# Performance work log

Measured on AMD Instinct MI355X. Metric: run time of the kernel, lower is better.

Reference implementation:

```python
import jax, jax.numpy as jnp
import numpy as np

EDGE_DROPOUT_RATE = 0.5  # RGCNEncoder edge_dropout_rate
DROPOUT_KEY = 42         # fixed key standing in for the encoder's dropout_key


def setup_inputs() -> dict:
    key = jax.random.key(0)
    ks = jax.random.split(key, 6)
    N, R, E, D, B, BI, BO = 100000, 16, 50000, 500, 100, 5, 5
    x = 0.01 * jax.random.normal(ks[0], (N, D), dtype=jnp.float32)  # pre_transform, normal() init (stddev=0.01)
    # block-decomposed relation weights: R relations x 100 blocks of 5x5
    w_rel1 = jax.random.normal(ks[1], (R, B, BI, BO), dtype=jnp.float32) / np.sqrt(BI)
    w_self1 = jax.random.normal(ks[2], (D, D), dtype=jnp.float32) / np.sqrt(D)
    w_rel2 = jax.random.normal(ks[3], (R, B, BI, BO), dtype=jnp.float32) / np.sqrt(BI)
    w_self2 = jax.random.normal(ks[4], (D, D), dtype=jnp.float32) / np.sqrt(D)
    edge_type_idcs = jax.random.randint(ks[5], (R, 2, E), 0, N, dtype=jnp.int32)
    edge_masks = jnp.ones((R, E), dtype=bool)
    return {"x": x, "w_rel1": w_rel1, "w_self1": w_self1,
            "w_rel2": w_rel2, "w_self2": w_self2,
            "edge_type_idcs": edge_type_idcs, "edge_masks": edge_masks}


def _rgcn_layer(h, w_rel, w_self, edge_type_idcs, edge_mask_f):
    """One block-decomposed RGCNConv with per-relation-node normalization + self loop."""
    N = h.shape[0]
    R, B, BI, BO = w_rel.shape
    Dout = B * BO
    out = h @ w_self  # self-connection
    for r in range(R):  # small fixed set of relations
        src = edge_type_idcs[r, 0]
        dst = edge_type_idcs[r, 1]
        mr = edge_mask_f[r]                              # [E]
        E = src.shape[0]
        hs = h[src].reshape(E, B, BI)                    # gather + split into blocks
        msg = jnp.einsum('ebi,bio->ebo', hs, w_rel[r]).reshape(E, Dout)
        msg = msg * mr[:, None]                          # masked (incl. edge dropout)
        agg = jax.ops.segment_sum(msg, dst, num_segments=N)   # [N, Dout]
        cnt = jax.ops.segment_sum(mr, dst, num_segments=N)    # per-relation in-degree
        out = out + agg / jnp.maximum(cnt, 1.0)[:, None]
    return jax.nn.relu(out)


def reference(x, w_rel1, w_self1, w_rel2, w_self2, edge_type_idcs, edge_masks):
    # edge dropout (all_data.dropout): keep each edge with prob 1 - rate
    keep = jax.random.bernoulli(jax.random.key(DROPOUT_KEY), 1.0 - EDGE_DROPOUT_RATE, edge_masks.shape)
    mask_f = (edge_masks & keep).astype(x.dtype)
    h = _rgcn_layer(x, w_rel1, w_self1, edge_type_idcs, mask_f)
    h = _rgcn_layer(h, w_rel2, w_self2, edge_type_idcs, mask_f)
    return h
```

## Files before the change

### kernel.cpp

```cpp
#include <hip/hip_runtime.h>
#include <hip/hip_bf16.h>
#include <stdint.h>

#define N_NODES 100000
#define N_REL   16
#define N_EDGE  50000
#define DIM     500
#define TOT_E   (N_REL * N_EDGE)
#define CNT_N   (N_REL * N_NODES)

#define INV_OFF    0ull
#define DEG_OFF    6400000ull
#define ROW_OFF    6800000ull
#define SCANP_OFF  7201000ull
#define CURS_OFF   7210000ull
#define ELIST_OFF  7610000ull
#define WB1_OFF    14020000ull
#define WB2_OFF    14550000ull
#define H1_OFF     15080000ull
#define WEXP1_OFF  115080000ull
#define WEXP2_OFF  115240000ull

typedef __attribute__((ext_vector_type(8))) short bf16x8;
typedef __attribute__((ext_vector_type(4))) float f32x4;

__device__ __forceinline__ uint32_t rotl32(uint32_t x, int d) {
    return (x << d) | (x >> (32 - d));
}
__device__ __forceinline__ bool edge_keep(uint32_t j) {
    uint32_t x0 = 0u, x1 = j;
    const uint32_t ks0 = 0u, ks1 = 42u, ks2 = 0u ^ 42u ^ 0x1BD11BDAu;
    const int RA[4] = {13, 15, 26, 6};
    const int RB[4] = {17, 29, 16, 24};
    x0 += ks0; x1 += ks1;
#pragma unroll
    for (int i = 0; i < 4; i++) { x0 += x1; x1 = rotl32(x1, RA[i]); x1 ^= x0; }
    x0 += ks1; x1 += ks2 + 1u;
#pragma unroll
    for (int i = 0; i < 4; i++) { x0 += x1; x1 = rotl32(x1, RB[i]); x1 ^= x0; }
    x0 += ks2; x1 += ks0 + 2u;
#pragma unroll
    for (int i = 0; i < 4; i++) { x0 += x1; x1 = rotl32(x1, RA[i]); x1 ^= x0; }
    x0 += ks0; x1 += ks1 + 3u;
#pragma unroll
    for (int i = 0; i < 4; i++) { x0 += x1; x1 = rotl32(x1, RB[i]); x1 ^= x0; }
    x0 += ks1; x1 += ks2 + 4u;
#pragma unroll
    for (int i = 0; i < 4; i++) { x0 += x1; x1 = rotl32(x1, RA[i]); x1 ^= x0; }
    x0 += ks2; x1 += ks0 + 5u;
    return ((x0 ^ x1) >> 31) == 0u;
}

__device__ __forceinline__ uint16_t f2bf(float f) {
    uint32_t u = __float_as_uint(f);
    u += 0x7FFFu + ((u >> 16) & 1u);
    return (uint16_t)(u >> 16);
}
__device__ __forceinline__ float bf2f(uint16_t v) {
    return __uint_as_float((uint32_t)v << 16);
}

__global__ __launch_bounds__(256) void zero_kernel(uint32_t* __restrict__ p, int n) {
    int t = blockIdx.x * blockDim.x + threadIdx.x;
    if (t < n) p[t] = 0u;
}

__global__ __launch_bounds__(256) void count_kernel(
        const int* __restrict__ eidx, uint32_t* __restrict__ cnt,
        uint32_t* __restrict__ deg) {
    int tid = blockIdx.x * blockDim.x + threadIdx.x;
    if (tid >= TOT_E) return;
    if (edge_keep((uint32_t)tid)) {
        int r = tid / N_EDGE;
        int e = tid - r * N_EDGE;
        int dst = eidx[(r * 2 + 1) * N_EDGE + e];
        atomicAdd(&cnt[r * N_NODES + dst], 1u);
        atomicAdd(&deg[dst], 1u);
    }
}

__global__ __launch_bounds__(256) void inv_kernel(uint32_t* __restrict__ cnt_u,
                                                  float* __restrict__ inv) {
    int t = blockIdx.x * blockDim.x + threadIdx.x;
    if (t < CNT_N) {
        float c = (float)cnt_u[t];
        inv[t] = 1.0f / fmaxf(c, 1.0f);
    }
}

__global__ __launch_bounds__(256) void scan1_kernel(
        const uint32_t* __restrict__ deg, uint32_t* __restrict__ rowptr,
        uint32_t* __restrict__ scanp) {
    __shared__ uint32_t sh[256];
    int b = blockIdx.x, t = threadIdx.x;
    int base = b * 1024 + t * 4;
    uint32_t x[4];
#pragma unroll
    for (int i = 0; i < 4; i++) x[i] = (base + i < N_NODES) ? deg[base + i] : 0u;
    uint32_t s = x[0] + x[1] + x[2] + x[3];
    sh[t] = s; __syncthreads();
    for (int off = 1; off < 256; off <<= 1) {
        uint32_t v = (t >= off) ? sh[t - off] : 0u;
        __syncthreads();
        sh[t] += v;
        __syncthreads();
    }
    uint32_t run = sh[t] - s;
    if (t == 255) scanp[b] = sh[255];
#pragma unroll
    for (int i = 0; i < 4; i++) {
        if (base + i < N_NODES) rowptr[base + i] = run;
        run += x[i];
    }
}

__global__ __launch_bounds__(128) void scan2_kernel(
        uint32_t* __restrict__ scanp, uint32_t* __restrict__ rowptr, int nb) {
    __shared__ uint32_t sh[128];
    int t = threadIdx.x;
    uint32_t v = (t < nb) ? scanp[t] : 0u;
    sh[t] = v; __syncthreads();
    for (int off = 1; off < 128; off <<= 1) {
        uint32_t u = (t >= off) ? sh[t - off] : 0u;
        __syncthreads();
        sh[t] += u;
        __syncthreads();
    }
    if (t < nb) scanp[t] = sh[t] - v;
    if (t == 127) rowptr[N_NODES] = sh[127];
}

__global__ __launch_bounds__(256) void scan3_kernel(
        uint32_t* __restrict__ rowptr, const uint32_t* __restrict__ scanp,
        uint32_t* __restrict__ curs) {
    int b = blockIdx.x, t = threadIdx.x;
    int base = b * 1024 + t * 4;
    uint32_t off = scanp[b];
#pragma unroll
    for (int i = 0; i < 4; i++) {
        int idx = base + i;
        if (idx < N_NODES) {
            uint32_t v = rowptr[idx] + off;
            rowptr[idx] = v;
            curs[idx] = v;
        }
    }
}

__global__ __launch_bounds__(256) void scatter_kernel(
        const int* __restrict__ eidx, const float* __restrict__ inv,
        uint32_t* __restrict__ curs, uint2* __restrict__ elist2) {
    int tid = blockIdx.x * blockDim.x + threadIdx.x;
    if (tid >= TOT_E) return;
    if (edge_keep((uint32_t)tid)) {
        int r = tid / N_EDGE;
        int e = tid - r * N_EDGE;
        int src = eidx[(r * 2 + 0) * N_EDGE + e];
        int dst = eidx[(r * 2 + 1) * N_EDGE + e];
        uint32_t pos = atomicAdd(&curs[dst], 1u);
        uint2 rec;
        rec.x = (uint32_t)src | ((uint32_t)r << 20);
        rec.y = __float_as_uint(inv[r * N_NODES + dst]);
        elist2[pos] = rec;
    }
}

__global__ __launch_bounds__(256) void conv_x_kernel(
        const float4* __restrict__ in, ushort4* __restrict__ outp, int n4) {
    int t = blockIdx.x * blockDim.x + threadIdx.x;
    if (t >= n4) return;
    float4 v = in[t];
    ushort4 o;
    o.x = f2bf(v.x); o.y = f2bf(v.y); o.z = f2bf(v.z); o.w = f2bf(v.w);
    outp[t] = o;
}

__global__ __launch_bounds__(256) void conv_w_kernel(
        const float* __restrict__ W, uint16_t* __restrict__ Bt) {
    int idx = blockIdx.x * 256 + threadIdx.x;
    int n = idx >> 9, k = idx & 511;
    float v = (n < DIM && k < DIM) ? W[k * DIM + n] : 0.f;
    Bt[idx] = f2bf(v);
}

__global__ __launch_bounds__(256) void conv_wexp_kernel(
        const float* __restrict__ W, float* __restrict__ wexp) {
    int idx = blockIdx.x * 256 + threadIdx.x;
    if (idx >= N_REL * 5 * DIM) return;
    int r = idx / (5 * DIM);
    int rem = idx - r * 5 * DIM;
    int i = rem / DIM;
    int j = rem - i * DIM;
    wexp[idx] = W[r * 2500 + (j / 5) * 25 + i * 5 + (j % 5)];
}

__global__ __launch_bounds__(256) void gemm_mfma_kernel(
        const uint16_t* __restrict__ A, const uint16_t* __restrict__ Bt,
        float* __restrict__ C, int M) {
    __shared__ uint16_t As[64][72];
    __shared__ uint16_t Bs[64][72];
    int m0 = blockIdx.x * 64;
    int n0 = blockIdx.y * 64;
    int t = threadIdx.x;
    int wave = t >> 6, lane = t & 63;
    int row_s = t >> 2;
    int k4 = (t & 3) * 16;
    f32x4 acc[4] = {};

    for (int k0 = 0; k0 < 512; k0 += 64) {
        {
            int gm = m0 + row_s;
            int gk = k0 + k4;
            uint16_t* dst = &As[row_s][k4];
            if (gm < M && gk + 15 < DIM) {
                *(bf16x8*)dst       = *(const bf16x8*)&A[(long)gm * DIM + gk];
                *(bf16x8*)(dst + 8) = *(const bf16x8*)&A[(long)gm * DIM + gk + 8];
            } else {
#pragma unroll
                for (int i = 0; i < 16; i++)
                    dst[i] = (gm < M && gk + i < DIM) ? A[(long)gm * DIM + gk + i] : (uint16_t)0;
            }
        }
        {
            uint16_t* dst = &Bs[row_s][k4];
            const uint16_t* srcp = &Bt[(n0 + row_s) * 512 + k0 + k4];
            *(bf16x8*)dst       = *(const bf16x8*)srcp;
            *(bf16x8*)(dst + 8) = *(const bf16x8*)(srcp + 8);
        }
        __syncthreads();

        int rA = (wave << 4) + (lane & 15);
        int ks = (lane >> 4) * 8;
        bf16x8 a0 = *(const bf16x8*)&As[rA][ks];
        bf16x8 a1 = *(const bf16x8*)&As[rA][32 + ks];
#pragma unroll
        for (int nt = 0; nt < 4; nt++) {
            int cB = (nt << 4) + (lane & 15);
            bf16x8 b0 = *(const bf16x8*)&Bs[cB][ks];
            bf16x8 b1 = *(const bf16x8*)&Bs[cB][32 + ks];
            acc[nt] = __builtin_amdgcn_mfma_f32_16x16x32_bf16(a0, b0, acc[nt], 0, 0, 0);
            acc[nt] = __builtin_amdgcn_mfma_f32_16x16x32_bf16(a1, b1, acc[nt], 0, 0, 0);
        }
        __syncthreads();
    }

    int rbase = m0 + (wave << 4) + ((lane >> 4) << 2);
    int cl = lane & 15;
#pragma unroll
    for (int nt = 0; nt < 4; nt++) {
        int col = n0 + (nt << 4) + cl;
        if (col < DIM) {
#pragma unroll
            for (int q = 0; q < 4; q++) {
                int rr = rbase + q;
                if (rr < M) C[(long)rr * DIM + col] = acc[nt][q];
            }
        }
    }
}

template <bool BF16H, bool OUT_BF16>
__global__ __launch_bounds__(256) void gather_kernel(
        const void* __restrict__ h, const float* __restrict__ wexp,
        const uint2* __restrict__ elist2, const uint32_t* __restrict__ rowptr,
        const float* __restrict__ self_in, float* __restrict__ out_f32,
        uint16_t* __restrict__ out_bf16) {
    int n = blockIdx.x;
    int wv = threadIdx.x >> 6, l = threadIdx.x & 63;
    const int D0 = wv * 125;
    const int j0 = l, j1 = l + 64;
    const bool has1 = (j1 < 125);
    const int b0 = j0 / 5;
    const int b1 = j1 / 5;

    __shared__ float hsb[4][2][128];

    uint32_t s = rowptr[n], e = rowptr[n + 1];
    float a0 = 0.f, a1 = 0.f;

    for (uint32_t p = s; p < e; p += 4) {
        const int k = (int)min(4u, e - p);
        uint2 rec[4];
#pragma unroll
        for (int i = 0; i < 4; i++) {
            if (i < k) rec[i] = elist2[p + i];
        }
        float v0[4], v1[4];
#pragma unroll
        for (int i = 0; i < 4; i++) {
            if (i < k) {
                uint32_t src = rec[i].x & 0xFFFFFu;
                if constexpr (BF16H) {
                    const uint16_t* row = (const uint16_t*)h + (size_t)src * DIM + D0;
                    v0[i] = bf2f(row[j0]);
                    v1[i] = has1 ? bf2f(row[j1]) : 0.f;
                } else {
                    const float* row = (const float*)h + (size_t)src * DIM + D0;
                    v0[i] = row[j0];
                    v1[i] = has1 ? row[j1] : 0.f;
                }
            }
        }
#pragma unroll
        for (int i = 0; i < 4; i++) {
            if (i < k) {
                float* hs = hsb[wv][i & 1];
                hs[j0] = v0[i];
                if (has1) hs[j1] = v1[i];
                uint32_t rl = rec[i].x >> 20;
                float inv = __uint_as_float(rec[i].y);
                const float* wbase = wexp + (size_t)rl * (5 * DIM) + D0;
                float w0[5];
#pragma unroll
                for (int q = 0; q < 5; q++) w0[q] = wbase[q * DIM + j0];
                const float* hp0 = hs + b0 * 5;
                float d0 = hp0[0] * w0[0] + hp0[1] * w0[1] + hp0[2] * w0[2]
                         + hp0[3] * w0[3] + hp0[4] * w0[4];
                a0 = fmaf(inv, d0, a0);
                if (has1) {
                    float w1[5];
#pragma unroll
                    for (int q = 0; q < 5; q++) w1[q] = wbase[q * DIM + j1];
                    const float* hp1 = hs + b1 * 5;
                    float d1 = hp1[0] * w1[0] + hp1[1] * w1[1] + hp1[2] * w1[2]
                             + hp1[3] * w1[3] + hp1[4] * w1[4];
                    a1 = fmaf(inv, d1, a1);
                }
            }
        }
    }

    long ob = (long)n * DIM + D0;
    {
        float v = fmaxf(self_in[ob + j0] + a0, 0.f);
        if (OUT_BF16) out_bf16[ob + j0] = f2bf(v);
        else          out_f32[ob + j0] = v;
    }
    if (has1) {
        float v = fmaxf(self_in[ob + j1] + a1, 0.f);
        if (OUT_BF16) out_bf16[ob + j1] = f2bf(v);
        else          out_f32[ob + j1] = v;
    }
}

extern "C" void kernel_launch(void* const* d_in, const int* in_sizes, int n_in,
                              void* d_out, int out_size, void* d_ws, size_t ws_size,
                              hipStream_t stream) {
    const float* x       = nullptr;
    const float* w_rel1  = nullptr;
    const float* w_rel2  = nullptr;
    const float* w_self1 = nullptr;
    const float* w_self2 = nullptr;
    const int*   eidx    = nullptr;
    for (int i = 0; i < n_in; i++) {
        int s = in_sizes[i];
        if (s == N_NODES * DIM) {
            x = (const float*)d_in[i];
        } else if (s == N_REL * 100 * 25) {
            if (!w_rel1) w_rel1 = (const float*)d_in[i];
            else         w_rel2 = (const float*)d_in[i];
        } else if (s == DIM * DIM) {
            if (!w_self1) w_self1 = (const float*)d_in[i];
            else          w_self2 = (const float*)d_in[i];
        } else if (s == N_REL * 2 * N_EDGE) {
            eidx = (const int*)d_in[i];
        }
    }
    float* out = (float*)d_out;

    char* ws = (char*)d_ws;
    uint32_t* cnt_u  = (uint32_t*)(ws + INV_OFF);
    float*    inv    = (float*)(ws + INV_OFF);
    uint32_t* deg    = (uint32_t*)(ws + DEG_OFF);
    uint32_t* rowptr = (uint32_t*)(ws + ROW_OFF);
    uint32_t* scanp  = (uint32_t*)(ws + SCANP_OFF);
    uint32_t* curs   = (uint32_t*)(ws + CURS_OFF);
    uint2*    elist2 = (uint2*)(ws + ELIST_OFF);
    uint16_t* wb1    = (uint16_t*)(ws + WB1_OFF);
    uint16_t* wb2    = (uint16_t*)(ws + WB2_OFF);
    uint16_t* h1     = (uint16_t*)(ws + H1_OFF);
    float*    wexp1  = (float*)(ws + WEXP1_OFF);
    float*    wexp2  = (float*)(ws + WEXP2_OFF);

    const int NB = (N_NODES + 1023) / 1024;

    zero_kernel<<<(CNT_N + N_NODES + 255) / 256, 256, 0, stream>>>(cnt_u, CNT_N + N_NODES);
    count_kernel<<<(TOT_E + 255) / 256, 256, 0, stream>>>(eidx, cnt_u, deg);
    inv_kernel<<<(CNT_N + 255) / 256, 256, 0, stream>>>(cnt_u, inv);
    scan1_kernel<<<NB, 256, 0, stream>>>(deg, rowptr, scanp);
    scan2_kernel<<<1, 128, 0, stream>>>(scanp, rowptr, NB);
    scan3_kernel<<<NB, 256, 0, stream>>>(rowptr, scanp, curs);
    scatter_kernel<<<(TOT_E + 255) / 256, 256, 0, stream>>>(eidx, inv, curs, elist2);

    conv_x_kernel<<<(N_NODES * DIM / 4 + 255) / 256, 256, 0, stream>>>(
        (const float4*)x, (ushort4*)h1, N_NODES * DIM / 4);
    conv_w_kernel<<<512 * 512 / 256, 256, 0, stream>>>(w_self1, wb1);
    conv_w_kernel<<<512 * 512 / 256, 256, 0, stream>>>(w_self2, wb2);
    conv_wexp_kernel<<<(N_REL * 5 * DIM + 255) / 256, 256, 0, stream>>>(w_rel1, wexp1);
    conv_wexp_kernel<<<(N_REL * 5 * DIM + 255) / 256, 256, 0, stream>>>(w_rel2, wexp2);

    dim3 ggrid((N_NODES + 63) / 64, 8);

    gemm_mfma_kernel<<<ggrid, 256, 0, stream>>>(h1, wb1, out, N_NODES);
    gather_kernel<false, true><<<N_NODES, 256, 0, stream>>>(
        x, wexp1, elist2, rowptr, out, nullptr, h1);

    gemm_mfma_kernel<<<ggrid, 256, 0, stream>>>(h1, wb2, out, N_NODES);
    gather_kernel<true, false><<<N_NODES, 256, 0, stream>>>(
        h1, wexp2, elist2, rowptr, out, out, nullptr);
}
```

Measured before the change: 1.225 ms.

## Enlarge self-GEMM tiles to 128x128 with 2x2 wave layout; prefetch self term

The dense self-connection GEMM now uses 128x128 output tiles, with each of four waves computing a 64x64 sub-tile as a 4x4 grid of MFMA fragments. This cuts how often A and B tiles are reloaded from global memory, raises the MFMA-to-load ratio, and halves the grid's column dimension. The cost is many more accumulator registers per thread and more LDS per block, which may lower occupancy. The gather kernel also loads its self-term value at the start so that load overlaps the edge loop.

```diff
diff --git a/kernel.cpp b/kernel.cpp
--- a/kernel.cpp
+++ b/kernel.cpp
@@ -194,66 +194,78 @@
     wexp[idx] = W[r * 2500 + (j / 5) * 25 + i * 5 + (j % 5)];
 }
 
-__global__ __launch_bounds__(256) void gemm_mfma_kernel(
+__global__ __launch_bounds__(256) void gemm_mfma128_kernel(
         const uint16_t* __restrict__ A, const uint16_t* __restrict__ Bt,
         float* __restrict__ C, int M) {
-    __shared__ uint16_t As[64][72];
-    __shared__ uint16_t Bs[64][72];
-    int m0 = blockIdx.x * 64;
-    int n0 = blockIdx.y * 64;
+    __shared__ uint16_t As[128][72];
+    __shared__ uint16_t Bs[128][72];
+    int m0 = blockIdx.x * 128;
+    int n0 = blockIdx.y * 128;
     int t = threadIdx.x;
     int wave = t >> 6, lane = t & 63;
-    int row_s = t >> 2;
-    int k4 = (t & 3) * 16;
-    f32x4 acc[4] = {};
+    int wm = wave >> 1, wn = wave & 1;
+    f32x4 acc[4][4] = {};
 
     for (int k0 = 0; k0 < 512; k0 += 64) {
-        {
-            int gm = m0 + row_s;
-            int gk = k0 + k4;
-            uint16_t* dst = &As[row_s][k4];
-            if (gm < M && gk + 15 < DIM) {
-                *(bf16x8*)dst       = *(const bf16x8*)&A[(long)gm * DIM + gk];
-                *(bf16x8*)(dst + 8) = *(const bf16x8*)&A[(long)gm * DIM + gk + 8];
+#pragma unroll
+        for (int i = 0; i < 4; i++) {
+            int c = t * 4 + i;
+            int row = c >> 3;
+            int col = (c & 7) * 8;
+            int gm = m0 + row, gk = k0 + col;
+            uint16_t* dst = &As[row][col];
+            if (gm < M && gk + 7 < DIM) {
+                *(bf16x8*)dst = *(const bf16x8*)&A[(size_t)gm * DIM + gk];
             } else {
 #pragma unroll
-                for (int i = 0; i < 16; i++)
-                    dst[i] = (gm < M && gk + i < DIM) ? A[(long)gm * DIM + gk + i] : (uint16_t)0;
+                for (int q = 0; q < 8; q++)
+                    dst[q] = (gm < M && gk + q < DIM) ? A[(size_t)gm * DIM + gk + q]
+                                                      : (uint16_t)0;
             }
-        }
-        {
-            uint16_t* dst = &Bs[row_s][k4];
-            const uint16_t* srcp = &Bt[(n0 + row_s) * 512 + k0 + k4];
-            *(bf16x8*)dst       = *(const bf16x8*)srcp;
-            *(bf16x8*)(dst + 8) = *(const bf16x8*)(srcp + 8);
-        }
-        __syncthreads();
-
-        int rA = (wave << 4) + (lane & 15);
+            *(bf16x8*)&Bs[row][col] =
+                *(const bf16x8*)&Bt[(size_t)(n0 + row) * 512 + k0 + col];
+        }
+        __syncthreads();
+
         int ks = (lane >> 4) * 8;
-        bf16x8 a0 = *(const bf16x8*)&As[rA][ks];
-        bf16x8 a1 = *(const bf16x8*)&As[rA][32 + ks];
+        int rl = lane & 15;
+        bf16x8 af[4][2], bfr[4][2];
+#pragma unroll
+        for (int mt = 0; mt < 4; mt++) {
+            af[mt][0] = *(const bf16x8*)&As[wm * 64 + mt * 16 + rl][ks];
+            af[mt][1] = *(const bf16x8*)&As[wm * 64 + mt * 16 + rl][32 + ks];
+        }
 #pragma unroll
         for (int nt = 0; nt < 4; nt++) {
-            int cB = (nt << 4) + (lane & 15);
-            bf16x8 b0 = *(const bf16x8*)&Bs[cB][ks];
-            bf16x8 b1 = *(const bf16x8*)&Bs[cB][32 + ks];
-            acc[nt] = __builtin_amdgcn_mfma_f32_16x16x32_bf16(a0, b0, acc[nt], 0, 0, 0);
-            acc[nt] = __builtin_amdgcn_mfma_f32_16x16x32_bf16(a1, b1, acc[nt], 0, 0, 0);
-        }
-        __syncthreads();
-    }
-
-    int rbase = m0 + (wave << 4) + ((lane >> 4) << 2);
+            bfr[nt][0] = *(const bf16x8*)&Bs[wn * 64 + nt * 16 + rl][ks];
+            bfr[nt][1] = *(const bf16x8*)&Bs[wn * 64 + nt * 16 + rl][32 + ks];
+        }
+#pragma unroll
+        for (int mt = 0; mt < 4; mt++)
+#pragma unroll
+            for (int nt = 0; nt < 4; nt++) {
+                acc[mt][nt] = __builtin_amdgcn_mfma_f32_16x16x32_bf16(
+                    af[mt][0], bfr[nt][0], acc[mt][nt], 0, 0, 0);
+                acc[mt][nt] = __builtin_amdgcn_mfma_f32_16x16x32_bf16(
+                    af[mt][1], bfr[nt][1], acc[mt][nt], 0, 0, 0);
+            }
+        __syncthreads();
+    }
+
     int cl = lane & 15;
-#pragma unroll
-    for (int nt = 0; nt < 4; nt++) {
-        int col = n0 + (nt << 4) + cl;
-        if (col < DIM) {
-#pragma unroll
-            for (int q = 0; q < 4; q++) {
-                int rr = rbase + q;
-                if (rr < M) C[(long)rr * DIM + col] = acc[nt][q];
+    int rq = (lane >> 4) << 2;
+#pragma unroll
+    for (int mt = 0; mt < 4; mt++) {
+        int rbase = m0 + wm * 64 + mt * 16 + rq;
+#pragma unroll
+        for (int nt = 0; nt < 4; nt++) {
+            int col = n0 + wn * 64 + nt * 16 + cl;
+            if (col < DIM) {
+#pragma unroll
+                for (int q = 0; q < 4; q++) {
+                    int rr = rbase + q;
+                    if (rr < M) C[(size_t)rr * DIM + col] = acc[mt][nt][q];
+                }
             }
         }
     }
@@ -275,6 +287,10 @@
 
     __shared__ float hsb[4][2][128];
 
+    long ob = (long)n * DIM + D0;
+    float self0 = self_in[ob + j0];
+    float self1 = has1 ? self_in[ob + j1] : 0.f;
+
     uint32_t s = rowptr[n], e = rowptr[n + 1];
     float a0 = 0.f, a1 = 0.f;
 
@@ -330,14 +346,13 @@
         }
     }
 
-    long ob = (long)n * DIM + D0;
     {
-        float v = fmaxf(self_in[ob + j0] + a0, 0.f);
+        float v = fmaxf(self0 + a0, 0.f);
         if (OUT_BF16) out_bf16[ob + j0] = f2bf(v);
         else          out_f32[ob + j0] = v;
     }
     if (has1) {
-        float v = fmaxf(self_in[ob + j1] + a1, 0.f);
+        float v = fmaxf(self1 + a1, 0.f);
         if (OUT_BF16) out_bf16[ob + j1] = f2bf(v);
         else          out_f32[ob + j1] = v;
     }
@@ -399,13 +414,13 @@
     conv_wexp_kernel<<<(N_REL * 5 * DIM + 255) / 256, 256, 0, stream>>>(w_rel1, wexp1);
     conv_wexp_kernel<<<(N_REL * 5 * DIM + 255) / 256, 256, 0, stream>>>(w_rel2, wexp2);
 
-    dim3 ggrid((N_NODES + 63) / 64, 8);
-
-    gemm_mfma_kernel<<<ggrid, 256, 0, stream>>>(h1, wb1, out, N_NODES);
+    dim3 ggrid((N_NODES + 127) / 128, 4);
+
+    gemm_mfma128_kernel<<<ggrid, 256, 0, stream>>>(h1, wb1, out, N_NODES);
     gather_kernel<false, true><<<N_NODES, 256, 0, stream>>>(
         x, wexp1, elist2, rowptr, out, nullptr, h1);
 
-    gemm_mfma_kernel<<<ggrid, 256, 0, stream>>>(h1, wb2, out, N_NODES);
+    gemm_mfma128_kernel<<<ggrid, 256, 0, stream>>>(h1, wb2, out, N_NODES);
     gather_kernel<true, false><<<N_NODES, 256, 0, stream>>>(
         h1, wexp2, elist2, rowptr, out, out, nullptr);
 }
```

Result: no change. 1.202 ms (-1.9%).
